# Optimization experiments

Hardware: AMD Instinct MI355X
Metric: run time of the kernel (lower is better)

Reference implementation:

```python
import jax, jax.numpy as jnp
import numpy as np

O_DIM, A_DIM, Z_DIM = 256, 8, 9
D, H, L, M, B = 128, 128, 4, 4, 65536  # module dim, MLP hidden, n_layers, n_modules, batch


def setup_inputs() -> dict:
    key = jax.random.key(0)
    ks = jax.random.split(key, 18)
    s = 0.05
    return {
        "o": jax.random.normal(ks[0], (B, O_DIM), jnp.float32),
        "z_map": jax.random.uniform(ks[1], (B, Z_DIM), jnp.float32),
        "collision_prob": jax.random.uniform(ks[2], (B, 1), jnp.float32),
        # base obs embedding and routing (task) embedding
        "Wb": jax.random.normal(ks[3], (O_DIM, D), jnp.float32) * s,
        "bb": jnp.zeros((D,), jnp.float32),
        "Wz": jax.random.normal(ks[4], (Z_DIM + 1, D), jnp.float32) * s,
        "bz": jnp.zeros((D,), jnp.float32),
        # L layers x M modules of DxD linears
        "Wm": jax.random.normal(ks[5], (L, M, D, D), jnp.float32) * s,
        "bm": jnp.zeros((L, M, D), jnp.float32),
        # routing heads: L-1 inter-layer (M*M) gates + final (M,) gate
        "Wg": jax.random.normal(ks[6], (L - 1, D, M * M), jnp.float32) * s,
        "Wg_last": jax.random.normal(ks[7], (D, M), jnp.float32) * s,
        # dueling heads
        "Wv": jax.random.normal(ks[8], (D, 1), jnp.float32) * s,
        "bv": jnp.zeros((1,), jnp.float32),
        "Wa1": jax.random.normal(ks[9], (D, H), jnp.float32) * s,
        "ba1": jnp.zeros((H,), jnp.float32),
        "Wa2": jax.random.normal(ks[10], (H, A_DIM), jnp.float32) * s,
        "ba2": jnp.zeros((A_DIM,), jnp.float32),
    }


def _softmodule(o, z_map, collision_prob, Wb, bb, Wz, bz, Wm, bm, Wg, Wg_last):
    f0 = jax.nn.relu(o @ Wb + bb)                              # (B, D)
    z_in = jnp.concatenate([z_map, collision_prob], axis=-1)   # (B, Z+1)
    g = jax.nn.relu(z_in @ Wz + bz) * f0                       # routing embedding (B, D)
    # layer 0: all modules consume the obs embedding
    x = jax.nn.relu(jnp.einsum("bd,mde->bme", f0, Wm[0]) + bm[0])  # (B, M, D)
    for l in range(1, L):
        logits = (g @ Wg[l - 1]).reshape(-1, M, M)             # (B, i, j)
        p = jax.nn.softmax(logits, axis=1)                     # soft routing over incoming modules i
        xin = jnp.einsum("bij,bid->bjd", p, x)                 # weighted gather-combine
        x = jax.nn.relu(jnp.einsum("bmd,mde->bme", xin, Wm[l]) + bm[l])
    p_last = jax.nn.softmax(g @ Wg_last, axis=-1)              # (B, M)
    return jnp.einsum("bm,bmd->bd", p_last, x)                 # (B, D)


def reference(o, z_map, collision_prob, Wb, bb, Wz, bz, Wm, bm, Wg, Wg_last,
              Wv, bv, Wa1, ba1, Wa2, ba2):
    feature = _softmodule(o, z_map, collision_prob, Wb, bb, Wz, bz, Wm, bm, Wg, Wg_last)
    value = feature @ Wv + bv                                  # (B, 1)
    adv = jax.nn.relu(feature @ Wa1 + ba1) @ Wa2 + ba2         # (B, A)
    adv = adv - adv.mean(axis=-1, keepdims=True)
    return adv + value
```

## Files before the change

kernel.cpp:

```cpp
#include <hip/hip_runtime.h>
#include <stdint.h>


typedef __attribute__((ext_vector_type(8))) short short8;
typedef __attribute__((ext_vector_type(4))) float f32x4;
typedef __attribute__((ext_vector_type(2))) float f32x2;
typedef __attribute__((address_space(1))) const unsigned int u32_g;
typedef __attribute__((address_space(3))) unsigned int u32_l;

__device__ __forceinline__ unsigned short f2bf(float f) {
  union { float f; uint32_t u; } v; v.f = f;
  uint32_t r = v.u + 0x7FFFu + ((v.u >> 16) & 1u);
  return (unsigned short)(r >> 16);
}
__device__ __forceinline__ float blo(uint32_t w) { union { uint32_t u; float f; } c; c.u = w << 16; return c.f; }
__device__ __forceinline__ float bhi(uint32_t w) { union { uint32_t u; float f; } c; c.u = w & 0xffff0000u; return c.f; }
__device__ __forceinline__ float b2f(unsigned short h) { union { uint32_t u; float f; } c; c.u = ((uint32_t)h) << 16; return c.f; }
__device__ __forceinline__ uint32_t cvtpk(float lo, float hi) {
  uint32_t d;
  asm("v_cvt_pk_bf16_f32 %0, %1, %2" : "=v"(d) : "v"(lo), "v"(hi));
  return d;
}
__device__ __forceinline__ f32x2 unpk2(uint32_t w) {
  f32x2 r; r.x = blo(w); r.y = bhi(w); return r;
}
union S8 { short8 s; uint32_t u[4]; };

__global__ void prep_weights(const float* __restrict__ Wb, const float* __restrict__ Wm,
                             const float* __restrict__ Wa1, const float* __restrict__ Wg,
                             const float* __restrict__ Wgl, const float* __restrict__ Wa2,
                             unsigned short* __restrict__ ws) {
  int idx = blockIdx.x * 256 + threadIdx.x;
  if (idx >= 321536) return;
  unsigned short v;
  if (idx < 32768) {
    int st = idx >> 12, q = (idx >> 10) & 3, n = (idx >> 3) & 127, kk = idx & 7;
    v = f2bf(Wb[(st * 32 + q * 8 + kk) * 128 + n]);
  } else if (idx < 40960) {
    int t = idx - 32768; int st = t >> 11, q = (t >> 9) & 3, n = (t >> 3) & 63, kk = t & 7;
    int k = st * 32 + q * 8 + kk;
    if (n < 48)      v = f2bf(Wg[(n >> 4) * 2048 + k * 16 + (n & 15)]);
    else if (n < 52) v = f2bf(Wgl[k * 4 + (n - 48)]);
    else             v = 0;
  } else if (idx < 303104) {
    int t = idx - 40960; int pg = t >> 12; int lj = pg >> 2, st = pg & 3;
    int q = (t >> 10) & 3, n = (t >> 3) & 127, kk = t & 7;
    v = f2bf(Wm[lj * 16384 + (st * 32 + q * 8 + kk) * 128 + n]);
  } else if (idx < 319488) {
    int t = idx - 303104; int st = t >> 12, q = (t >> 10) & 3, n = (t >> 3) & 127, kk = t & 7;
    v = f2bf(Wa1[(st * 32 + q * 8 + kk) * 128 + n]);
  } else {
    int t = idx - 319488; int st = t >> 9, q = (t >> 7) & 3, n = (t >> 3) & 15, kk = t & 7;
    int k = st * 32 + q * 8 + kk;
    v = (n < 8) ? f2bf(Wa2[k * 8 + n]) : (unsigned short)0;
  }
  ws[idx] = v;
}

__device__ __forceinline__ void gld16(const void* g, void* l) {
  __builtin_amdgcn_global_load_lds((u32_g*)g, (u32_l*)l, 16, 0, 0);
}

__device__ __forceinline__ void gemm32(const short8 xst, const unsigned short* C,
                                       int q, int ml, f32x4 a[8]) {
#pragma unroll
  for (int nt = 0; nt < 8; ++nt) {
    short8 bf = *(const short8*)(C + q * 1024 + (nt * 16 + ml) * 8);
    a[nt] = __builtin_amdgcn_mfma_f32_16x16x32_bf16(xst, bf, a[nt], 0, 0, 0);
  }
}
__device__ __forceinline__ void ldx4(const unsigned short* xbw, int q, int ml, short8 f[4]) {
#pragma unroll
  for (int st = 0; st < 4; ++st) f[st] = *(const short8*)(xbw + ml * 136 + st * 32 + q * 8);
}

__device__ __forceinline__ void combine_layer(const short8 xo[4][4],
                                              const unsigned short* __restrict__ prow,
                                              short8 xin[4][4]) {
  float p[4][4];
#pragma unroll
  for (int j = 0; j < 4; ++j) {
    uint32_t pw0 = *(const uint32_t*)(prow + j * 4);
    uint32_t pw1 = *(const uint32_t*)(prow + j * 4 + 2);
    p[j][0] = blo(pw0); p[j][1] = bhi(pw0); p[j][2] = blo(pw1); p[j][3] = bhi(pw1);
  }
#pragma unroll
  for (int st = 0; st < 4; ++st) {
    S8 x0, x1, x2, x3;
    x0.s = xo[0][st]; x1.s = xo[1][st]; x2.s = xo[2][st]; x3.s = xo[3][st];
    S8 r0, r1, r2, r3;
#pragma unroll
    for (int w = 0; w < 4; ++w) {
      f32x2 u0 = unpk2(x0.u[w]), u1 = unpk2(x1.u[w]), u2 = unpk2(x2.u[w]), u3 = unpk2(x3.u[w]);
      f32x2 s0 = p[0][0] * u0 + p[0][1] * u1 + p[0][2] * u2 + p[0][3] * u3;
      f32x2 s1 = p[1][0] * u0 + p[1][1] * u1 + p[1][2] * u2 + p[1][3] * u3;
      f32x2 s2 = p[2][0] * u0 + p[2][1] * u1 + p[2][2] * u2 + p[2][3] * u3;
      f32x2 s3 = p[3][0] * u0 + p[3][1] * u1 + p[3][2] * u2 + p[3][3] * u3;
      r0.u[w] = cvtpk(s0.x, s0.y); r1.u[w] = cvtpk(s1.x, s1.y);
      r2.u[w] = cvtpk(s2.x, s2.y); r3.u[w] = cvtpk(s3.x, s3.y);
    }
    xin[0][st] = r0.s; xin[1][st] = r1.s; xin[2][st] = r2.s; xin[3][st] = r3.s;
  }
}

#define RSYNC1() asm volatile("s_waitcnt vmcnt(1) lgkmcnt(0)\n\ts_barrier" ::: "memory")
#define RSYNC0() asm volatile("s_waitcnt vmcnt(0) lgkmcnt(0)\n\ts_barrier" ::: "memory")
#define RSTEP1(PTR) do { RSYNC1(); ring_issue(); (PTR) = ring_next(); } while (0)
#define RSTEP0(PTR) do { RSYNC0(); ring_issue(); (PTR) = ring_next(); } while (0)

__global__ __attribute__((amdgpu_flat_work_group_size(512, 512), amdgpu_waves_per_eu(2)))
void dueling_fused(
    const float* __restrict__ o, const float* __restrict__ zmap, const float* __restrict__ coll,
    const float* __restrict__ bb, const float* __restrict__ Wz, const float* __restrict__ bz,
    const float* __restrict__ bm, const float* __restrict__ Wv, const float* __restrict__ bv,
    const float* __restrict__ ba1, const float* __restrict__ ba2,
    const unsigned short* __restrict__ ws, float* __restrict__ out)
{
  __shared__ __align__(16) unsigned char smem[77824];
  unsigned short* xbuf  = (unsigned short*)(smem + 24576);
  unsigned short* pall  = (unsigned short*)(smem + 59392);
  float*          zbufF = (float*)(smem + 59392);
  float*          plast = (float*)(smem + 71680);
  float*          vbuf  = (float*)(smem + 71680);
  unsigned short* bmL   = (unsigned short*)(smem + 73728);

  const int tid = threadIdx.x;
  const int wv  = tid >> 6;
  const int lane = tid & 63;
  const int q   = lane >> 4;
  const int ml  = lane & 15;
  const int row0 = blockIdx.x * 128;
  unsigned short* xbw = xbuf + wv * 2176;

  for (int i = tid; i < 1280; i += 512) {
    if (i < 1152) { int r = i / 9, c = i - r * 9; zbufF[r * 12 + c] = zmap[(row0 + r) * 9 + c]; }
    else          { int r = i - 1152; zbufF[r * 12 + 9] = coll[row0 + r]; }
  }
  for (int i = tid; i < 2048; i += 512) bmL[i] = f2bf(bm[i]);

  short8 of[8];
  const float* orow = o + (size_t)(row0 + wv * 16 + ml) * 256;
#pragma unroll
  for (int st = 0; st < 8; ++st) {
    float4 v0 = *(const float4*)(orow + st * 32 + q * 8);
    float4 v1 = *(const float4*)(orow + st * 32 + q * 8 + 4);
    S8 af;
    af.u[0] = cvtpk(v0.x, v0.y); af.u[1] = cvtpk(v0.z, v0.w);
    af.u[2] = cvtpk(v1.x, v1.y); af.u[3] = cvtpk(v1.z, v1.w);
    of[st] = af.s;
  }
  asm volatile("s_waitcnt vmcnt(0) lgkmcnt(0)" ::: "memory");

  int r_kiss = 0, r_riss = 0, r_rc = 0;
  const char* r_gsrc = (const char*)ws;
  const int wld  = wv << 10;
  const int ln16 = (tid & 63) << 4;
  auto ring_issue = [&]() {
    if (r_kiss <= 78) {
      char* l = (char*)smem + r_riss;
      int soff = (r_kiss == 78) ? (wld & 4095) : wld;
      gld16(r_gsrc + soff + ln16, l + wld + ln16);
      r_gsrc += 8192;
    }
    ++r_kiss;
    r_riss += 8192; if (r_riss == 24576) r_riss = 0;
  };
  auto ring_next = [&]() -> const unsigned short* {
    const unsigned short* p = (const unsigned short*)(smem + r_rc);
    r_rc += 8192; if (r_rc == 24576) r_rc = 0;
    return p;
  };
  ring_issue(); ring_issue();

  const f32x4 z4 = {0.f, 0.f, 0.f, 0.f};
  const unsigned short* C;

  f32x4 acc[8];
#pragma unroll
  for (int nt = 0; nt < 8; ++nt) acc[nt] = z4;
#pragma unroll
  for (int st = 0; st < 8; ++st) { RSTEP1(C); gemm32(of[st], C, q, ml, acc); }
#pragma unroll
  for (int nt = 0; nt < 8; ++nt) {
    float bbv = bb[nt * 16 + ml];
#pragma unroll
    for (int r2 = 0; r2 < 4; ++r2) {
      float v = fmaxf(acc[nt][r2] + bbv, 0.f);
      acc[nt][r2] = v;
      xbw[(q * 4 + r2) * 136 + nt * 16 + ml] = f2bf(v);
    }
  }
  short8 f0f[4];
  ldx4(xbw, q, ml, f0f);

#pragma unroll
  for (int nt = 0; nt < 8; ++nt) {
    int col = nt * 16 + ml;
    float wz[10];
#pragma unroll
    for (int k = 0; k < 10; ++k) wz[k] = Wz[k * 128 + col];
    float bzv = bz[col];
#pragma unroll
    for (int r2 = 0; r2 < 4; ++r2) {
      int row = wv * 16 + q * 4 + r2;
      float zd = bzv;
#pragma unroll
      for (int k = 0; k < 10; ++k) zd += zbufF[row * 12 + k] * wz[k];
      xbw[(q * 4 + r2) * 136 + col] = f2bf(fmaxf(zd, 0.f) * acc[nt][r2]);
    }
  }
  short8 gf[4];
  ldx4(xbw, q, ml, gf);

  f32x4 ag[4];
#pragma unroll
  for (int nt = 0; nt < 4; ++nt) ag[nt] = z4;
  RSTEP0(C);
#pragma unroll
  for (int sp = 0; sp < 2; ++sp)
#pragma unroll
    for (int nt = 0; nt < 4; ++nt) {
      short8 bf = *(const short8*)(C + sp * 2048 + q * 512 + (nt * 16 + ml) * 8);
      ag[nt] = __builtin_amdgcn_mfma_f32_16x16x32_bf16(gf[sp], bf, ag[nt], 0, 0, 0);
    }
  RSTEP1(C);
#pragma unroll
  for (int sp = 0; sp < 2; ++sp)
#pragma unroll
    for (int nt = 0; nt < 4; ++nt) {
      short8 bf = *(const short8*)(C + sp * 2048 + q * 512 + (nt * 16 + ml) * 8);
      ag[nt] = __builtin_amdgcn_mfma_f32_16x16x32_bf16(gf[2 + sp], bf, ag[nt], 0, 0, 0);
    }
#pragma unroll
  for (int li = 0; li < 3; ++li) {
#pragma unroll
    for (int r2 = 0; r2 < 4; ++r2) {
      float a = ag[li][r2];
      float m = fmaxf(a, __shfl_xor(a, 4)); m = fmaxf(m, __shfl_xor(m, 8));
      float e = __expf(a - m);
      float s = e; s += __shfl_xor(s, 4); s += __shfl_xor(s, 8);
      pall[(li * 128 + wv * 16 + q * 4 + r2) * 16 + (ml & 3) * 4 + (ml >> 2)] = f2bf(e / s);
    }
  }
#pragma unroll
  for (int r2 = 0; r2 < 4; ++r2) {
    float a = ag[3][r2];
    float m = fmaxf(a, __shfl_xor(a, 1)); m = fmaxf(m, __shfl_xor(m, 2));
    float e = __expf(a - m);
    float s = e; s += __shfl_xor(s, 1); s += __shfl_xor(s, 2);
    if (ml < 4) plast[(wv * 16 + q * 4 + r2) * 4 + ml] = e / s;
  }

  short8 xo[4][4];
  f32x4 a[8];
#pragma unroll
  for (int j = 0; j < 4; ++j) {
    if (j > 0) ldx4(xbw, q, ml, xo[j - 1]);
#pragma unroll
    for (int nt = 0; nt < 8; ++nt) a[nt] = z4;
#pragma unroll
    for (int st = 0; st < 4; ++st) { RSTEP1(C); gemm32(f0f[st], C, q, ml, a); }
#pragma unroll
    for (int nt = 0; nt < 8; ++nt) {
      float bmv = b2f(bmL[j * 128 + nt * 16 + ml]);
#pragma unroll
      for (int r2 = 0; r2 < 4; ++r2)
        xbw[(q * 4 + r2) * 136 + nt * 16 + ml] = f2bf(fmaxf(a[nt][r2] + bmv, 0.f));
    }
  }

  short8 xin[4][4];
  for (int l = 1; l <= 2; ++l) {
    ldx4(xbw, q, ml, xo[3]);
    combine_layer(xo, pall + ((l - 1) * 128 + wv * 16 + ml) * 16, xin);
#pragma unroll
    for (int j = 0; j < 4; ++j) {
      if (j > 0) ldx4(xbw, q, ml, xo[j - 1]);
#pragma unroll
      for (int nt = 0; nt < 8; ++nt) a[nt] = z4;
#pragma unroll
      for (int st = 0; st < 4; ++st) { RSTEP1(C); gemm32(xin[j][st], C, q, ml, a); }
#pragma unroll
      for (int nt = 0; nt < 8; ++nt) {
        float bmv = b2f(bmL[(l * 4 + j) * 128 + nt * 16 + ml]);
#pragma unroll
        for (int r2 = 0; r2 < 4; ++r2)
          xbw[(q * 4 + r2) * 136 + nt * 16 + ml] = f2bf(fmaxf(a[nt][r2] + bmv, 0.f));
      }
    }
  }

  f32x4 feat[8];
  {
    ldx4(xbw, q, ml, xo[3]);
    combine_layer(xo, pall + (2 * 128 + wv * 16 + ml) * 16, xin);
#pragma unroll
    for (int nt = 0; nt < 8; ++nt) feat[nt] = z4;
#pragma unroll
    for (int j = 0; j < 4; ++j) {
#pragma unroll
      for (int nt = 0; nt < 8; ++nt) a[nt] = z4;
#pragma unroll
      for (int st = 0; st < 4; ++st) { RSTEP1(C); gemm32(xin[j][st], C, q, ml, a); }
      float pl[4];
#pragma unroll
      for (int r2 = 0; r2 < 4; ++r2) pl[r2] = plast[(wv * 16 + q * 4 + r2) * 4 + j];
#pragma unroll
      for (int nt = 0; nt < 8; ++nt) {
        float bmv = b2f(bmL[(12 + j) * 128 + nt * 16 + ml]);
#pragma unroll
        for (int r2 = 0; r2 < 4; ++r2)
          feat[nt][r2] += pl[r2] * fmaxf(a[nt][r2] + bmv, 0.f);
      }
    }
  }

#pragma unroll
  for (int nt = 0; nt < 8; ++nt)
#pragma unroll
    for (int r2 = 0; r2 < 4; ++r2)
      xbw[(q * 4 + r2) * 136 + nt * 16 + ml] = f2bf(feat[nt][r2]);
  short8 ff[4];
  ldx4(xbw, q, ml, ff);
#pragma unroll
  for (int nt = 0; nt < 8; ++nt) a[nt] = z4;
#pragma unroll
  for (int st = 0; st < 4; ++st) { RSTEP1(C); gemm32(ff[st], C, q, ml, a); }

  {
    float wvv[8];
#pragma unroll
    for (int nt = 0; nt < 8; ++nt) wvv[nt] = Wv[nt * 16 + ml];
    float bvv = bv[0];
#pragma unroll
    for (int r2 = 0; r2 < 4; ++r2) {
      float v = 0.f;
#pragma unroll
      for (int nt = 0; nt < 8; ++nt) v += feat[nt][r2] * wvv[nt];
      v += __shfl_xor(v, 1); v += __shfl_xor(v, 2); v += __shfl_xor(v, 4); v += __shfl_xor(v, 8);
      if (ml == 0) vbuf[wv * 16 + q * 4 + r2] = v + bvv;
    }
  }

#pragma unroll
  for (int nt = 0; nt < 8; ++nt) {
    float b1v = ba1[nt * 16 + ml];
#pragma unroll
    for (int r2 = 0; r2 < 4; ++r2)
      xbw[(q * 4 + r2) * 136 + nt * 16 + ml] = f2bf(fmaxf(a[nt][r2] + b1v, 0.f));
  }
  short8 a1f[4];
  ldx4(xbw, q, ml, a1f);

  RSTEP0(C);
  f32x4 av = z4;
#pragma unroll
  for (int st = 0; st < 4; ++st) {
    short8 bf = *(const short8*)(C + st * 512 + q * 128 + ml * 8);
    av = __builtin_amdgcn_mfma_f32_16x16x32_bf16(a1f[st], bf, av, 0, 0, 0);
  }
  float ba2v = ba2[ml & 7];
#pragma unroll
  for (int r2 = 0; r2 < 4; ++r2) {
    float aa = av[r2] + ba2v;
    float s = aa + __shfl_xor(aa, 1); s += __shfl_xor(s, 2); s += __shfl_xor(s, 4);
    if (ml < 8)
      out[(size_t)(row0 + wv * 16 + q * 4 + r2) * 8 + ml] = aa - s * 0.125f + vbuf[wv * 16 + q * 4 + r2];
  }
}

extern "C" void kernel_launch(void* const* d_in, const int* in_sizes, int n_in,
                              void* d_out, int out_size, void* d_ws, size_t ws_size,
                              hipStream_t stream) {
  const float* o   = (const float*)d_in[0];
  const float* zm  = (const float*)d_in[1];
  const float* cp  = (const float*)d_in[2];
  const float* Wb  = (const float*)d_in[3];
  const float* bb  = (const float*)d_in[4];
  const float* Wz  = (const float*)d_in[5];
  const float* bz  = (const float*)d_in[6];
  const float* Wm  = (const float*)d_in[7];
  const float* bm  = (const float*)d_in[8];
  const float* Wg  = (const float*)d_in[9];
  const float* Wgl = (const float*)d_in[10];
  const float* Wv  = (const float*)d_in[11];
  const float* bv  = (const float*)d_in[12];
  const float* Wa1 = (const float*)d_in[13];
  const float* ba1 = (const float*)d_in[14];
  const float* Wa2 = (const float*)d_in[15];
  const float* ba2 = (const float*)d_in[16];
  unsigned short* wsT = (unsigned short*)d_ws;

  int B = in_sizes[0] / 256;

  hipLaunchKernelGGL(prep_weights, dim3(1256), dim3(256), 0, stream,
                     Wb, Wm, Wa1, Wg, Wgl, Wa2, wsT);
  hipLaunchKernelGGL(dueling_fused, dim3(B / 128), dim3(512), 0, stream,
                     o, zm, cp, bb, Wz, bz, bm, Wv, bv, ba1, ba2,
                     wsT, (float*)d_out);
}
```

Before: 220.4 us.

## Read MFMA weight fragments directly from global memory instead of LDS ring

Removes the three-slot LDS ring buffer that streamed weight chunks with global_load_lds and a barrier per step. Each wave now loads B-operand fragments straight from the pre-packed global workspace, which should hit in L2/L1 since every block reads the same weights. This drops the per-step block-wide barriers and shrinks LDS use, possibly allowing more resident blocks. The cost is more global load traffic and latency exposed directly to the MFMA chain, with no software prefetch.

```diff
diff --git a/kernel.cpp b/kernel.cpp
--- a/kernel.cpp
+++ b/kernel.cpp
@@ -5,8 +5,6 @@
 typedef __attribute__((ext_vector_type(8))) short short8;
 typedef __attribute__((ext_vector_type(4))) float f32x4;
 typedef __attribute__((ext_vector_type(2))) float f32x2;
-typedef __attribute__((address_space(1))) const unsigned int u32_g;
-typedef __attribute__((address_space(3))) unsigned int u32_l;
 
 __device__ __forceinline__ unsigned short f2bf(float f) {
   union { float f; uint32_t u; } v; v.f = f;
@@ -57,12 +55,8 @@
   ws[idx] = v;
 }
 
-__device__ __forceinline__ void gld16(const void* g, void* l) {
-  __builtin_amdgcn_global_load_lds((u32_g*)g, (u32_l*)l, 16, 0, 0);
-}
-
-__device__ __forceinline__ void gemm32(const short8 xst, const unsigned short* C,
-                                       int q, int ml, f32x4 a[8]) {
+__device__ __forceinline__ void gemmG(const short8 xst, const unsigned short* __restrict__ C,
+                                      int q, int ml, f32x4 a[8]) {
 #pragma unroll
   for (int nt = 0; nt < 8; ++nt) {
     short8 bf = *(const short8*)(C + q * 1024 + (nt * 16 + ml) * 8);
@@ -103,11 +97,6 @@
   }
 }
 
-#define RSYNC1() asm volatile("s_waitcnt vmcnt(1) lgkmcnt(0)\n\ts_barrier" ::: "memory")
-#define RSYNC0() asm volatile("s_waitcnt vmcnt(0) lgkmcnt(0)\n\ts_barrier" ::: "memory")
-#define RSTEP1(PTR) do { RSYNC1(); ring_issue(); (PTR) = ring_next(); } while (0)
-#define RSTEP0(PTR) do { RSYNC0(); ring_issue(); (PTR) = ring_next(); } while (0)
-
 __global__ __attribute__((amdgpu_flat_work_group_size(512, 512), amdgpu_waves_per_eu(2)))
 void dueling_fused(
     const float* __restrict__ o, const float* __restrict__ zmap, const float* __restrict__ coll,
@@ -116,13 +105,13 @@
     const float* __restrict__ ba1, const float* __restrict__ ba2,
     const unsigned short* __restrict__ ws, float* __restrict__ out)
 {
-  __shared__ __align__(16) unsigned char smem[77824];
-  unsigned short* xbuf  = (unsigned short*)(smem + 24576);
-  unsigned short* pall  = (unsigned short*)(smem + 59392);
-  float*          zbufF = (float*)(smem + 59392);
-  float*          plast = (float*)(smem + 71680);
-  float*          vbuf  = (float*)(smem + 71680);
-  unsigned short* bmL   = (unsigned short*)(smem + 73728);
+  __shared__ __align__(16) unsigned char smem[53760];
+  unsigned short* xbuf  = (unsigned short*)(smem);
+  unsigned short* pall  = (unsigned short*)(smem + 34816);
+  float*          zbufF = (float*)(smem + 34816);
+  float*          plast = (float*)(smem + 47104);
+  float*          vbuf  = (float*)(smem + 49152);
+  unsigned short* bmL   = (unsigned short*)(smem + 49664);
 
   const int tid = threadIdx.x;
   const int wv  = tid >> 6;
@@ -149,37 +138,15 @@
     af.u[2] = cvtpk(v1.x, v1.y); af.u[3] = cvtpk(v1.z, v1.w);
     of[st] = af.s;
   }
-  asm volatile("s_waitcnt vmcnt(0) lgkmcnt(0)" ::: "memory");
-
-  int r_kiss = 0, r_riss = 0, r_rc = 0;
-  const char* r_gsrc = (const char*)ws;
-  const int wld  = wv << 10;
-  const int ln16 = (tid & 63) << 4;
-  auto ring_issue = [&]() {
-    if (r_kiss <= 78) {
-      char* l = (char*)smem + r_riss;
-      int soff = (r_kiss == 78) ? (wld & 4095) : wld;
-      gld16(r_gsrc + soff + ln16, l + wld + ln16);
-      r_gsrc += 8192;
-    }
-    ++r_kiss;
-    r_riss += 8192; if (r_riss == 24576) r_riss = 0;
-  };
-  auto ring_next = [&]() -> const unsigned short* {
-    const unsigned short* p = (const unsigned short*)(smem + r_rc);
-    r_rc += 8192; if (r_rc == 24576) r_rc = 0;
-    return p;
-  };
-  ring_issue(); ring_issue();
+  __syncthreads();
 
   const f32x4 z4 = {0.f, 0.f, 0.f, 0.f};
-  const unsigned short* C;
 
   f32x4 acc[8];
 #pragma unroll
   for (int nt = 0; nt < 8; ++nt) acc[nt] = z4;
 #pragma unroll
-  for (int st = 0; st < 8; ++st) { RSTEP1(C); gemm32(of[st], C, q, ml, acc); }
+  for (int st = 0; st < 8; ++st) gemmG(of[st], ws + st * 4096, q, ml, acc);
 #pragma unroll
   for (int nt = 0; nt < 8; ++nt) {
     float bbv = bb[nt * 16 + ml];
@@ -211,26 +178,29 @@
   }
   short8 gf[4];
   ldx4(xbw, q, ml, gf);
+  __syncthreads();
 
   f32x4 ag[4];
 #pragma unroll
   for (int nt = 0; nt < 4; ++nt) ag[nt] = z4;
-  RSTEP0(C);
-#pragma unroll
-  for (int sp = 0; sp < 2; ++sp)
-#pragma unroll
-    for (int nt = 0; nt < 4; ++nt) {
-      short8 bf = *(const short8*)(C + sp * 2048 + q * 512 + (nt * 16 + ml) * 8);
-      ag[nt] = __builtin_amdgcn_mfma_f32_16x16x32_bf16(gf[sp], bf, ag[nt], 0, 0, 0);
-    }
-  RSTEP1(C);
-#pragma unroll
-  for (int sp = 0; sp < 2; ++sp)
-#pragma unroll
-    for (int nt = 0; nt < 4; ++nt) {
-      short8 bf = *(const short8*)(C + sp * 2048 + q * 512 + (nt * 16 + ml) * 8);
-      ag[nt] = __builtin_amdgcn_mfma_f32_16x16x32_bf16(gf[2 + sp], bf, ag[nt], 0, 0, 0);
-    }
+  {
+    const unsigned short* C8 = ws + 8 * 4096;
+    const unsigned short* C9 = ws + 9 * 4096;
+#pragma unroll
+    for (int sp = 0; sp < 2; ++sp)
+#pragma unroll
+      for (int nt = 0; nt < 4; ++nt) {
+        short8 bf = *(const short8*)(C8 + sp * 2048 + q * 512 + (nt * 16 + ml) * 8);
+        ag[nt] = __builtin_amdgcn_mfma_f32_16x16x32_bf16(gf[sp], bf, ag[nt], 0, 0, 0);
+      }
+#pragma unroll
+    for (int sp = 0; sp < 2; ++sp)
+#pragma unroll
+      for (int nt = 0; nt < 4; ++nt) {
+        short8 bf = *(const short8*)(C9 + sp * 2048 + q * 512 + (nt * 16 + ml) * 8);
+        ag[nt] = __builtin_amdgcn_mfma_f32_16x16x32_bf16(gf[2 + sp], bf, ag[nt], 0, 0, 0);
+      }
+  }
 #pragma unroll
   for (int li = 0; li < 3; ++li) {
 #pragma unroll
@@ -259,7 +229,7 @@
 #pragma unroll
     for (int nt = 0; nt < 8; ++nt) a[nt] = z4;
 #pragma unroll
-    for (int st = 0; st < 4; ++st) { RSTEP1(C); gemm32(f0f[st], C, q, ml, a); }
+    for (int st = 0; st < 4; ++st) gemmG(f0f[st], ws + (10 + j * 4 + st) * 4096, q, ml, a);
 #pragma unroll
     for (int nt = 0; nt < 8; ++nt) {
       float bmv = b2f(bmL[j * 128 + nt * 16 + ml]);
@@ -279,7 +249,8 @@
 #pragma unroll
       for (int nt = 0; nt < 8; ++nt) a[nt] = z4;
 #pragma unroll
-      for (int st = 0; st < 4; ++st) { RSTEP1(C); gemm32(xin[j][st], C, q, ml, a); }
+      for (int st = 0; st < 4; ++st)
+        gemmG(xin[j][st], ws + (10 + (l * 4 + j) * 4 + st) * 4096, q, ml, a);
 #pragma unroll
       for (int nt = 0; nt < 8; ++nt) {
         float bmv = b2f(bmL[(l * 4 + j) * 128 + nt * 16 + ml]);
@@ -301,7 +272,8 @@
 #pragma unroll
       for (int nt = 0; nt < 8; ++nt) a[nt] = z4;
 #pragma unroll
-      for (int st = 0; st < 4; ++st) { RSTEP1(C); gemm32(xin[j][st], C, q, ml, a); }
+      for (int st = 0; st < 4; ++st)
+        gemmG(xin[j][st], ws + (58 + j * 4 + st) * 4096, q, ml, a);
       float pl[4];
 #pragma unroll
       for (int r2 = 0; r2 < 4; ++r2) pl[r2] = plast[(wv * 16 + q * 4 + r2) * 4 + j];
@@ -325,7 +297,7 @@
 #pragma unroll
   for (int nt = 0; nt < 8; ++nt) a[nt] = z4;
 #pragma unroll
-  for (int st = 0; st < 4; ++st) { RSTEP1(C); gemm32(ff[st], C, q, ml, a); }
+  for (int st = 0; st < 4; ++st) gemmG(ff[st], ws + (74 + st) * 4096, q, ml, a);
 
   {
     float wvv[8];
@@ -352,11 +324,11 @@
   short8 a1f[4];
   ldx4(xbw, q, ml, a1f);
 
-  RSTEP0(C);
+  const unsigned short* C78 = ws + 78 * 4096;
   f32x4 av = z4;
 #pragma unroll
   for (int st = 0; st < 4; ++st) {
-    short8 bf = *(const short8*)(C + st * 512 + q * 128 + ml * 8);
+    short8 bf = *(const short8*)(C78 + st * 512 + q * 128 + ml * 8);
     av = __builtin_amdgcn_mfma_f32_16x16x32_bf16(a1f[st], bf, av, 0, 0, 0);
   }
   float ba2v = ba2[ml & 7];
```

Result: slower. 393.1 us (+78.4%).
